# Performance work log

Measured on AMD Instinct MI355X. Metric: run time of the kernel, lower is better.

Reference implementation:

```python
import jax, jax.numpy as jnp
import numpy as np
from jax import lax

WINDOW_SIZE = 5
GRAD_THRESH = 0.15
MAX_ITER = 5
EPS = 1e-8


def setup_inputs() -> dict:
    key = jax.random.key(0)
    k1, k2, k3 = jax.random.split(key, 3)
    B, M, T = 16, 128, 12000
    return {
        "mel_features": jax.random.normal(k1, (B, M, T), jnp.float32),
        "spectral_features": jax.random.normal(k2, (B, T), jnp.float32),
        "initial_boundaries": jax.random.uniform(k3, (B, T), dtype=jnp.float32),
        "similarity_weights": jnp.ones(3, jnp.float32) / 3.0,
    }


def _consistency_scores(mel, spec, weights):
    # mel: (B, M, T), spec: (B, T), weights: (3,)
    B, M, T = mel.shape
    # cosine similarity between consecutive frames (vectorized over t)
    a, b = mel[:, :, :-1], mel[:, :, 1:]
    dot = jnp.sum(a * b, axis=1)
    na = jnp.sqrt(jnp.sum(a * a, axis=1))
    nb = jnp.sqrt(jnp.sum(b * b, axis=1))
    cos = dot / (jnp.maximum(na, EPS) * jnp.maximum(nb, EPS))  # (B, T-1)
    mel_sim = jnp.pad(cos, ((0, 0), (1, 0)))  # t=0 stays 0 (torch init zeros)

    spec_diff = jnp.abs(spec[:, 1:] - spec[:, :-1])
    spec_sim = jnp.pad(1.0 / (1.0 + spec_diff), ((0, 0), (1, 0)), constant_values=1.0)

    # avg_pool1d(mean over mel bins, k, stride=1, pad=k//2, count_include_pad)
    k = min(WINDOW_SIZE, T)
    mean_mel = jnp.mean(mel, axis=1)  # (B, T)
    pad = k // 2
    padded = jnp.pad(mean_mel, ((0, 0), (pad, pad)))
    cs = jnp.pad(jnp.cumsum(padded, axis=1), ((0, 0), (1, 0)))
    smooth = (cs[:, k:] - cs[:, :-k]) / k  # (B, T)
    # torch.std default is unbiased (ddof=1)
    temporal = 1.0 - jnp.std(smooth, axis=1, ddof=1, keepdims=True)  # (B, 1)
    temporal = jnp.broadcast_to(temporal, (B, T))

    return weights[0] * mel_sim + weights[1] * spec_sim + weights[2] * temporal


def _adjustments(candidates, cons):
    # local mean of cons over [t-2, t+3) clipped to [0, T)
    B, T = cons.shape
    cs = jnp.pad(jnp.cumsum(cons, axis=1), ((0, 0), (1, 0)))  # (B, T+1)
    t = jnp.arange(T)
    lo = jnp.maximum(t - 2, 0)
    hi = jnp.minimum(t + 3, T)
    local = (cs[:, hi] - cs[:, lo]) / (hi - lo).astype(cons.dtype)
    interior = (t >= 1) & (t <= T - 2)  # loop ran over range(1, T-1)
    active = (candidates > 0.5) & interior
    return jnp.where(active & (local > 0.7), -0.1,
                     jnp.where(active & (local < 0.4), 0.1, 0.0)).astype(cons.dtype)


def reference(mel_features, spectral_features, initial_boundaries, similarity_weights):
    weights = jax.nn.softmax(similarity_weights)
    cons = _consistency_scores(mel_features, spectral_features, weights)
    # gradient-based candidates are fixed across iterations (cons is fixed)
    grads = jnp.pad(jnp.abs(cons[:, 1:] - cons[:, :-1]), ((0, 0), (1, 0)))
    cand_static = (grads > GRAD_THRESH).astype(cons.dtype)

    def body(carry, _):
        refined, done = carry
        candidates = jnp.maximum(cand_static, refined)
        adj = _adjustments(candidates, cons)
        adj = jnp.where(done, 0.0, adj)  # replicate early break by freezing
        new_refined = jnp.clip(refined + adj, 0.0, 1.0)
        new_done = done | (jnp.sum(jnp.abs(adj)) < 0.01)
        return (new_refined, new_done), None

    (refined, _), _ = lax.scan(body, (initial_boundaries, jnp.array(False)),
                               None, length=MAX_ITER)
    return refined
```

## Files before the change

### kernel.cpp

```cpp
#include <hip/hip_runtime.h>
#include <cstdint>

#define BB 16
#define MM 128
#define TT 12000
constexpr int BT = BB * TT;

__global__ void k1_colstats(const float* __restrict__ mel,
                            float* __restrict__ ssq,
                            float* __restrict__ dotv,
                            float* __restrict__ cmean,
                            unsigned int* __restrict__ counts) {
    if (blockIdx.x == 0 && blockIdx.y == 0 && threadIdx.x < 8)
        counts[threadIdx.x] = 0u;
    const int b = blockIdx.y;
    const int t = blockIdx.x * blockDim.x + threadIdx.x;
    if (t >= TT) return;
    const float* base = mel + (size_t)b * MM * TT;
    float accd = 0.f, accq = 0.f, accs = 0.f;
    {
#pragma clang fp contract(off)
        for (int m = 0; m < MM; ++m) {
            const float* rowp = base + (size_t)m * TT;
            float cur = rowp[t];
            float prev = (t > 0) ? rowp[t - 1] : 0.f;
            accd += prev * cur;
            accq += cur * cur;
            accs += cur;
        }
    }
    size_t i = (size_t)b * TT + t;
    ssq[i] = accq; dotv[i] = accd; cmean[i] = accs * (1.0f / MM);
}

__global__ void kA_temporal(const float* __restrict__ cmean,
                            float* __restrict__ temporal) {
    const int b = blockIdx.x;
    const int tid = threadIdx.x;
    __shared__ __align__(16) float row_s[TT];
    __shared__ float red[256];
    __shared__ float mean_s;
    const float4* c4 = (const float4*)(cmean + (size_t)b * TT);
    float4* r4 = (float4*)row_s;
    for (int i = tid; i < TT / 4; i += 256) r4[i] = c4[i];
    __syncthreads();

    float s = 0.f;
    for (int t = tid; t < TT; t += 256) {
        float v = 0.f;
        int lo = t - 2 < 0 ? 0 : t - 2;
        int hi = t + 2 >= TT ? TT - 1 : t + 2;
        for (int j = lo; j <= hi; ++j) v += row_s[j];
        s += v / 5.0f;
    }
    red[tid] = s; __syncthreads();
    for (int o = 128; o > 0; o >>= 1) {
        if (tid < o) red[tid] += red[tid + o];
        __syncthreads();
    }
    if (tid == 0) mean_s = red[0] / (float)TT;
    __syncthreads();
    float mean = mean_s;
    float ss = 0.f;
    for (int t = tid; t < TT; t += 256) {
        float v = 0.f;
        int lo = t - 2 < 0 ? 0 : t - 2;
        int hi = t + 2 >= TT ? TT - 1 : t + 2;
        for (int j = lo; j <= hi; ++j) v += row_s[j];
        float sm = v / 5.0f - mean;
        ss += sm * sm;
    }
    red[tid] = ss; __syncthreads();
    for (int o = 128; o > 0; o >>= 1) {
        if (tid < o) red[tid] += red[tid + o];
        __syncthreads();
    }
    if (tid == 0) {
        float var = red[0] / (float)(TT - 1);
        temporal[b] = 1.0f - sqrtf(var);
    }
}

__global__ void kB_cons(const float* __restrict__ ssq,
                        const float* __restrict__ dotv,
                        const float* __restrict__ spec,
                        const float* __restrict__ temporal,
                        const float* __restrict__ wraw,
                        float* __restrict__ cons) {
    const int idx = blockIdx.x * 256 + threadIdx.x;
    const int b = idx / TT;
    const int t = idx - b * TT;
    float x0 = wraw[0], x1 = wraw[1], x2 = wraw[2];
    float mx = fmaxf(x0, fmaxf(x1, x2));
    float e0 = expf(x0 - mx), e1 = expf(x1 - mx), e2 = expf(x2 - mx);
    float es = (e0 + e1) + e2;
    float w0 = e0 / es, w1 = e1 / es, w2 = e2 / es;
    float mel_sim, spec_sim;
    if (t == 0) { mel_sim = 0.f; spec_sim = 1.f; }
    else {
        float na = fmaxf(sqrtf(ssq[idx - 1]), 1e-8f);
        float nb = fmaxf(sqrtf(ssq[idx]),     1e-8f);
        float den = na * nb; asm volatile("" : "+v"(den));
        mel_sim = dotv[idx] / den;
        float d = fabsf(spec[idx] - spec[idx - 1]);
        spec_sim = 1.0f / (1.0f + d);
    }
    float pa = w0 * mel_sim;     asm volatile("" : "+v"(pa));
    float pb = w1 * spec_sim;    asm volatile("" : "+v"(pb));
    float pc = w2 * temporal[b]; asm volatile("" : "+v"(pc));
    cons[idx] = (pa + pb) + pc;
}

#define ADD4(P, R0, R1, R2, R3) \
    "v_add_f32 v" R0 ", v" P  ", v" R0 "\n\t" \
    "v_add_f32 v" R1 ", v" R0 ", v" R1 "\n\t" \
    "v_add_f32 v" R2 ", v" R1 ", v" R2 "\n\t" \
    "v_add_f32 v" R3 ", v" R2 ", v" R3 "\n\t"

#define SBW(Q0a,Q0b,Q0c,Q0d, Q1a,Q1b,Q1c,Q1d, Q2a,Q2b,Q2c,Q2d, Q3a,Q3b,Q3c,Q3d, O0,O1,O2,O3, W) \
    "s_waitcnt lgkmcnt(" W ")\n\t" \
    ADD4("43", Q0a, Q0b, Q0c, Q0d) \
    ADD4(Q0d,  Q1a, Q1b, Q1c, Q1d) \
    ADD4(Q1d,  Q2a, Q2b, Q2c, Q2d) \
    ADD4(Q2d,  Q3a, Q3b, Q3c, Q3d) \
    "v_mov_b32 v43, v" Q3d "\n\t" \
    "ds_write_b128 v41, v[" Q0a ":" Q0d "] offset:" O0 "\n\t" \
    "ds_write_b128 v41, v[" Q1a ":" Q1d "] offset:" O1 "\n\t" \
    "ds_write_b128 v41, v[" Q2a ":" Q2d "] offset:" O2 "\n\t" \
    "ds_write_b128 v41, v[" Q3a ":" Q3d "] offset:" O3 "\n\t" \
    "ds_read_b128 v[" Q0a ":" Q0d "], v40 offset:" O0 "\n\t" \
    "ds_read_b128 v[" Q1a ":" Q1d "], v40 offset:" O1 "\n\t" \
    "ds_read_b128 v[" Q2a ":" Q2d "], v40 offset:" O2 "\n\t" \
    "ds_read_b128 v[" Q3a ":" Q3d "], v40 offset:" O3 "\n\t"

#define SBW_A(O_W, W) SBW("44","45","46","47","48","49","50","51", \
                          "52","53","54","55","56","57","58","59", \
                          "0","16","32","48", W)
#define SBW_B(W)      SBW("60","61","62","63","64","65","66","67", \
                          "68","69","70","71","72","73","74","75", \
                          "64","80","96","112", W)

__global__ void __launch_bounds__(256)
kC_row(const float* __restrict__ cons,
       float* __restrict__ CSg) {
    const int b = blockIdx.x;
    const int tid = threadIdx.x;
    __shared__ __align__(16) float buf[TT + 64];

    const float4* c4 = (const float4*)(cons + (size_t)b * TT);
    float4* b4 = (float4*)buf;
    for (int i = tid; i < TT / 4; i += 256) b4[i] = c4[i];
    __syncthreads();

    if (tid == 0) {
        uint32_t lds_base = (uint32_t)(uintptr_t)&buf[0];
        asm volatile(
            "v_mov_b32 v41, %0\n\t"
            "v_add_u32 v40, 128, v41\n\t"
            "v_mov_b32 v43, 0\n\t"
            "ds_read_b128 v[44:47], v41\n\t"
            "ds_read_b128 v[48:51], v41 offset:16\n\t"
            "ds_read_b128 v[52:55], v41 offset:32\n\t"
            "ds_read_b128 v[56:59], v41 offset:48\n\t"
            "ds_read_b128 v[60:63], v41 offset:64\n\t"
            "ds_read_b128 v[64:67], v41 offset:80\n\t"
            "ds_read_b128 v[68:71], v41 offset:96\n\t"
            "ds_read_b128 v[72:75], v41 offset:112\n\t"
            SBW_A("0", "4")
            SBW_B("8")
            "v_add_u32 v40, 128, v40\n\t"
            "v_add_u32 v41, 128, v41\n\t"
            "s_mov_b32 s20, 374\n\t"
            "3:\n\t"
            SBW_A("0", "8")
            SBW_B("8")
            "v_add_u32 v40, 128, v40\n\t"
            "v_add_u32 v41, 128, v41\n\t"
            "s_sub_u32 s20, s20, 1\n\t"
            "s_cmp_lg_u32 s20, 0\n\t"
            "s_cbranch_scc1 3b\n\t"
            "s_waitcnt lgkmcnt(0)\n\t"
            :
            : "v"(lds_base)
            : "v40", "v41", "v43",
              "v44", "v45", "v46", "v47", "v48", "v49", "v50", "v51",
              "v52", "v53", "v54", "v55", "v56", "v57", "v58", "v59",
              "v60", "v61", "v62", "v63", "v64", "v65", "v66", "v67",
              "v68", "v69", "v70", "v71", "v72", "v73", "v74", "v75",
              "s20", "scc", "memory");
    }
    __syncthreads();

    float4* cs4 = (float4*)(CSg + (size_t)b * TT);
    for (int i = tid; i < TT / 4; i += 256) cs4[i] = b4[i];
}

__global__ void kD_prepare(const float* __restrict__ cons,
                           const float* __restrict__ CSg,
                           const float* __restrict__ init,
                           float* __restrict__ stepv,
                           float* __restrict__ candf,
                           unsigned int* __restrict__ counts) {
    const int idx = blockIdx.x * 256 + threadIdx.x;
    const int b = idx / TT;
    const int t = idx - b * TT;
    __shared__ unsigned sflag[5];
    if (threadIdx.x < 5) sflag[threadIdx.x] = 0u;
    __syncthreads();

    const float* csr = CSg + (size_t)b * TT;
    int lo = t - 2; if (lo < 0) lo = 0;
    int hi = t + 3; if (hi > TT) hi = TT;
    float csH = csr[hi - 1];
    float csL = (lo > 0) ? csr[lo - 1] : 0.f;
    float local = (csH - csL) / (float)(hi - lo);
    float dir = (local > 0.7f) ? -0.1f : ((local < 0.4f) ? 0.1f : 0.0f);
    bool interior = (t >= 1) && (t <= TT - 2);
    float step = interior ? dir : 0.0f;
    float g = (t == 0) ? 0.f : fabsf(cons[idx] - cons[idx - 1]);
    float cand = (g > 0.15f) ? 1.f : 0.f;
    float r = init[idx];
    bool nz[5];
#pragma unroll
    for (int j = 0; j < 5; ++j) {
        float adj = (fmaxf(cand, r) > 0.5f) ? step : 0.0f;
        nz[j] = (adj != 0.0f);
        r = fminf(fmaxf(r + adj, 0.0f), 1.0f);
    }
    stepv[idx] = step; candf[idx] = cand;
    const int lane = threadIdx.x & 63;
#pragma unroll
    for (int j = 0; j < 5; ++j) {
        unsigned long long mb = __ballot(nz[j]);
        if (lane == 0 && mb) atomicOr(&sflag[j], 1u);
    }
    __syncthreads();
    if (threadIdx.x < 5 && sflag[threadIdx.x]) counts[threadIdx.x] = 1u;
}

__global__ void k_final(const float* __restrict__ init,
                        const float* __restrict__ stepv,
                        const float* __restrict__ candf,
                        const unsigned int* __restrict__ counts,
                        float* __restrict__ outp) {
    const int idx = blockIdx.x * 256 + threadIdx.x;
    float r = init[idx];
    float step = stepv[idx];
    float cand = candf[idx];
    unsigned c[5];
#pragma unroll
    for (int j = 0; j < 5; ++j) c[j] = counts[j];
#pragma unroll
    for (int j = 0; j < 5; ++j) {
        if (c[j] == 0u) break;
        float adj = (fmaxf(cand, r) > 0.5f) ? step : 0.0f;
        r = fminf(fmaxf(r + adj, 0.0f), 1.0f);
    }
    outp[idx] = r;
}

extern "C" void kernel_launch(void* const* d_in, const int* in_sizes, int n_in,
                              void* d_out, int out_size, void* d_ws, size_t ws_size,
                              hipStream_t stream) {
    const float* mel  = (const float*)d_in[0];
    const float* spec = (const float*)d_in[1];
    const float* init = (const float*)d_in[2];
    const float* wts  = (const float*)d_in[3];

    float* ws = (float*)d_ws;
    float* ssq   = ws;
    float* dotv  = ws + 192000;
    float* cmean = ws + 384000;
    float* cons  = ws + 576000;
    float* CSg   = ws + 768000;
    float* stepv = ws + 960000;
    float* candf = ws + 1152000;
    float* temporal = ws + 1344000;
    unsigned int* counts = (unsigned int*)(ws + 1344016);

    dim3 g1((TT + 255) / 256, BB);
    k1_colstats<<<g1, 256, 0, stream>>>(mel, ssq, dotv, cmean, counts);
    kA_temporal<<<BB, 256, 0, stream>>>(cmean, temporal);
    kB_cons<<<BT / 256, 256, 0, stream>>>(ssq, dotv, spec, temporal, wts, cons);
    kC_row<<<BB, 256, 0, stream>>>(cons, CSg);
    kD_prepare<<<BT / 256, 256, 0, stream>>>(cons, CSg, init, stepv, candf, counts);
    k_final<<<BT / 256, 256, 0, stream>>>(init, stepv, candf, counts, (float*)d_out);
}
```

Measured before the change: 145.9 us.

## Replace LDS-staged single-thread row scan with direct global streaming prefix sum

```diff
diff --git a/kernel.cpp b/kernel.cpp
--- a/kernel.cpp
+++ b/kernel.cpp
@@ -111,88 +111,32 @@
     cons[idx] = (pa + pb) + pc;
 }
 
-#define ADD4(P, R0, R1, R2, R3) \
-    "v_add_f32 v" R0 ", v" P  ", v" R0 "\n\t" \
-    "v_add_f32 v" R1 ", v" R0 ", v" R1 "\n\t" \
-    "v_add_f32 v" R2 ", v" R1 ", v" R2 "\n\t" \
-    "v_add_f32 v" R3 ", v" R2 ", v" R3 "\n\t"
-
-#define SBW(Q0a,Q0b,Q0c,Q0d, Q1a,Q1b,Q1c,Q1d, Q2a,Q2b,Q2c,Q2d, Q3a,Q3b,Q3c,Q3d, O0,O1,O2,O3, W) \
-    "s_waitcnt lgkmcnt(" W ")\n\t" \
-    ADD4("43", Q0a, Q0b, Q0c, Q0d) \
-    ADD4(Q0d,  Q1a, Q1b, Q1c, Q1d) \
-    ADD4(Q1d,  Q2a, Q2b, Q2c, Q2d) \
-    ADD4(Q2d,  Q3a, Q3b, Q3c, Q3d) \
-    "v_mov_b32 v43, v" Q3d "\n\t" \
-    "ds_write_b128 v41, v[" Q0a ":" Q0d "] offset:" O0 "\n\t" \
-    "ds_write_b128 v41, v[" Q1a ":" Q1d "] offset:" O1 "\n\t" \
-    "ds_write_b128 v41, v[" Q2a ":" Q2d "] offset:" O2 "\n\t" \
-    "ds_write_b128 v41, v[" Q3a ":" Q3d "] offset:" O3 "\n\t" \
-    "ds_read_b128 v[" Q0a ":" Q0d "], v40 offset:" O0 "\n\t" \
-    "ds_read_b128 v[" Q1a ":" Q1d "], v40 offset:" O1 "\n\t" \
-    "ds_read_b128 v[" Q2a ":" Q2d "], v40 offset:" O2 "\n\t" \
-    "ds_read_b128 v[" Q3a ":" Q3d "], v40 offset:" O3 "\n\t"
-
-#define SBW_A(O_W, W) SBW("44","45","46","47","48","49","50","51", \
-                          "52","53","54","55","56","57","58","59", \
-                          "0","16","32","48", W)
-#define SBW_B(W)      SBW("60","61","62","63","64","65","66","67", \
-                          "68","69","70","71","72","73","74","75", \
-                          "64","80","96","112", W)
-
-__global__ void __launch_bounds__(256)
-kC_row(const float* __restrict__ cons,
-       float* __restrict__ CSg) {
-    const int b = blockIdx.x;
-    const int tid = threadIdx.x;
-    __shared__ __align__(16) float buf[TT + 64];
-
-    const float4* c4 = (const float4*)(cons + (size_t)b * TT);
-    float4* b4 = (float4*)buf;
-    for (int i = tid; i < TT / 4; i += 256) b4[i] = c4[i];
-    __syncthreads();
-
-    if (tid == 0) {
-        uint32_t lds_base = (uint32_t)(uintptr_t)&buf[0];
-        asm volatile(
-            "v_mov_b32 v41, %0\n\t"
-            "v_add_u32 v40, 128, v41\n\t"
-            "v_mov_b32 v43, 0\n\t"
-            "ds_read_b128 v[44:47], v41\n\t"
-            "ds_read_b128 v[48:51], v41 offset:16\n\t"
-            "ds_read_b128 v[52:55], v41 offset:32\n\t"
-            "ds_read_b128 v[56:59], v41 offset:48\n\t"
-            "ds_read_b128 v[60:63], v41 offset:64\n\t"
-            "ds_read_b128 v[64:67], v41 offset:80\n\t"
-            "ds_read_b128 v[68:71], v41 offset:96\n\t"
-            "ds_read_b128 v[72:75], v41 offset:112\n\t"
-            SBW_A("0", "4")
-            SBW_B("8")
-            "v_add_u32 v40, 128, v40\n\t"
-            "v_add_u32 v41, 128, v41\n\t"
-            "s_mov_b32 s20, 374\n\t"
-            "3:\n\t"
-            SBW_A("0", "8")
-            SBW_B("8")
-            "v_add_u32 v40, 128, v40\n\t"
-            "v_add_u32 v41, 128, v41\n\t"
-            "s_sub_u32 s20, s20, 1\n\t"
-            "s_cmp_lg_u32 s20, 0\n\t"
-            "s_cbranch_scc1 3b\n\t"
-            "s_waitcnt lgkmcnt(0)\n\t"
-            :
-            : "v"(lds_base)
-            : "v40", "v41", "v43",
-              "v44", "v45", "v46", "v47", "v48", "v49", "v50", "v51",
-              "v52", "v53", "v54", "v55", "v56", "v57", "v58", "v59",
-              "v60", "v61", "v62", "v63", "v64", "v65", "v66", "v67",
-              "v68", "v69", "v70", "v71", "v72", "v73", "v74", "v75",
-              "s20", "scc", "memory");
-    }
-    __syncthreads();
-
-    float4* cs4 = (float4*)(CSg + (size_t)b * TT);
-    for (int i = tid; i < TT / 4; i += 256) cs4[i] = b4[i];
+__global__ void __launch_bounds__(64)
+kC_scan16(const float* __restrict__ cons,
+          float* __restrict__ CSg) {
+    const int r = threadIdx.x;
+    if (r >= BB) return;
+    const float4* __restrict__ in4  = (const float4*)(cons + (size_t)r * TT);
+    float4* __restrict__ out4       = (float4*)(CSg  + (size_t)r * TT);
+    constexpr int NG = TT / 4;
+    constexpr int PF = 30;
+    float4 ring[PF];
+#pragma unroll
+    for (int k = 0; k < PF; ++k) ring[k] = in4[k];
+    float acc = 0.f;
+    for (int g = 0; g < NG; g += PF) {
+#pragma unroll
+        for (int k = 0; k < PF; ++k) {
+            float4 v = ring[k];
+            int src = g + PF + k;
+            ring[k] = in4[src < NG ? src : NG - 1];
+            acc += v.x; v.x = acc;
+            acc += v.y; v.y = acc;
+            acc += v.z; v.z = acc;
+            acc += v.w; v.w = acc;
+            out4[g + k] = v;
+        }
+    }
 }
 
 __global__ void kD_prepare(const float* __restrict__ cons,
@@ -282,7 +226,7 @@
     k1_colstats<<<g1, 256, 0, stream>>>(mel, ssq, dotv, cmean, counts);
     kA_temporal<<<BB, 256, 0, stream>>>(cmean, temporal);
     kB_cons<<<BT / 256, 256, 0, stream>>>(ssq, dotv, spec, temporal, wts, cons);
-    kC_row<<<BB, 256, 0, stream>>>(cons, CSg);
+    kC_scan16<<<1, 64, 0, stream>>>(cons, CSg);
     kD_prepare<<<BT / 256, 256, 0, stream>>>(cons, CSg, init, stepv, candf, counts);
     k_final<<<BT / 256, 256, 0, stream>>>(init, stepv, candf, counts, (float*)d_out);
 }
```

New measurement: 165.6 us. 13.5% more time.
